# Kernel tuning notes

Hardware: AMD Instinct MI355X
Metric: run time of the kernel (lower is better)

## Reference

```python
import jax, jax.numpy as jnp
import numpy as np

B, SQ, SK, H, NH = 2, 2048, 2048, 2048, 16
HD = H // NH  # 128
NEG = -1e9


def setup_inputs() -> dict:
    key = jax.random.key(0)
    ks = jax.random.split(key, 8)
    hidden_states = jax.random.normal(ks[0], (B, SQ, H), dtype=jnp.float32)
    # key already transposed/expanded for baddbmm: [B*nh, head_dim, key_len]
    k = jax.random.normal(ks[1], (B * NH, HD, SK), dtype=jnp.float32)
    v = jax.random.normal(ks[2], (B, NH, SK, HD), dtype=jnp.float32)
    # additive float causal mask [B, 1, Sq, Sk]
    causal = jnp.tril(jnp.ones((SQ, SK), dtype=bool))
    attention_mask = jnp.where(causal, 0.0, NEG).astype(jnp.float32)
    attention_mask = jnp.broadcast_to(attention_mask[None, None], (B, 1, SQ, SK))
    w_q = jax.random.normal(ks[3], (H, H), dtype=jnp.float32) * 0.02
    b_q = jnp.zeros((H,), dtype=jnp.float32)
    w_proj = jax.random.normal(ks[4], (H, H), dtype=jnp.float32) * 0.02
    b_proj = jnp.zeros((H,), dtype=jnp.float32)
    return {
        "hidden_states": hidden_states,
        "key": k,
        "value": v,
        "attention_mask": attention_mask,
        "w_q": w_q,
        "b_q": b_q,
        "w_proj": w_proj,
        "b_proj": b_proj,
    }


def reference(hidden_states, key, value, attention_mask, w_q, b_q, w_proj, b_proj):
    dtype = hidden_states.dtype
    scale = 1.0 / (HD ** 0.5)  # scale_attn_weights=True, attention_multiplier=None
    # q projection: [B, Sq, H] -> [B, nh, Sq, hd]
    q = hidden_states @ w_q.T + b_q
    q = q.reshape(B, SQ, NH, HD).transpose(0, 2, 1, 3)
    # key comes in as [B*nh, hd, Sk]
    k = key.reshape(B, NH, HD, SK)
    # scores = mask + scale * q @ k  (baddbmm with beta=1)
    scores = attention_mask + scale * jnp.einsum("bhqd,bhdk->bhqk", q, k)
    # softmax in fp32 (attention_softmax_in_fp32=True), cast back
    probs = jax.nn.softmax(scores.astype(jnp.float32), axis=-1).astype(dtype)
    # attn_pdrop=0 -> no dropout
    out = jnp.einsum("bhqk,bhkd->bhqd", probs, value)  # [B, nh, Sq, hd]
    out = out.transpose(0, 2, 1, 3).reshape(B, SQ, H)
    out = out @ w_proj.T + b_proj  # resid_pdrop=0 -> no dropout
    return out
```

## Files before the change

kernel.cpp:

```cpp
#include <hip/hip_runtime.h>
#include <hip/hip_bf16.h>

typedef __bf16 bf16;
typedef __bf16 bf16x4 __attribute__((ext_vector_type(4)));
typedef __bf16 bf16x8 __attribute__((ext_vector_type(8)));
typedef float  f32x4  __attribute__((ext_vector_type(4)));
typedef float  f32x16 __attribute__((ext_vector_type(16)));
typedef unsigned int u32;

#define B_   2
#define SQ_  2048
#define SK_  2048
#define H_   2048
#define NH_  16
#define HD_  128
#define BH_  (B_*NH_)

__device__ inline void gl_lds16(const bf16* g, bf16* l) {
  __builtin_amdgcn_global_load_lds(
      (const __attribute__((address_space(1))) u32*)(const void*)g,
      (__attribute__((address_space(3))) u32*)(void*)l,
      16, 0, 0);
}

__device__ inline float exp2_fast(float x) {
  float r; asm("v_exp_f32 %0, %1" : "=v"(r) : "v"(x)); return r;
}

union PW { u32 w[4]; bf16x8 v; };

__global__ __launch_bounds__(256) void cvt3_f32_bf16(const float* __restrict__ a, bf16* __restrict__ ao,
                                                     const float* __restrict__ b, bf16* __restrict__ bo,
                                                     const float* __restrict__ c, bf16* __restrict__ co) {
  const int blk = blockIdx.x;
  const float* in; bf16* out; int n4, bstart, nblk;
  if (blk < 1024)      { in = a; out = ao; n4 = (B_ * SQ_ * H_) / 4; bstart = 0;    nblk = 1024; }
  else if (blk < 1536) { in = b; out = bo; n4 = (H_ * H_) / 4;       bstart = 1024; nblk = 512; }
  else                 { in = c; out = co; n4 = (H_ * H_) / 4;       bstart = 1536; nblk = 512; }
  int i = (blk - bstart) * 256 + threadIdx.x;
  const int stride = nblk * 256;
  for (; i < n4; i += stride) {
    float4 v = ((const float4*)in)[i];
    bf16x4 w; w[0] = (bf16)v.x; w[1] = (bf16)v.y; w[2] = (bf16)v.z; w[3] = (bf16)v.w;
    ((bf16x4*)out)[i] = w;
  }
}

__global__ __launch_bounds__(256) void transpose_cvt2(const float* __restrict__ key,
                                                      const float* __restrict__ value,
                                                      bf16* __restrict__ kout,
                                                      bf16* __restrict__ vout) {
  __shared__ float tile[64][65];
  const int id = blockIdx.x;
  const float* src; bf16* dst; int R, C, r0, c0, bh;
  if (id < 2048) {
    src = key; dst = kout; R = HD_; C = SK_;
    c0 = (id & 31) * 64; r0 = ((id >> 5) & 1) * 64; bh = id >> 6;
  } else {
    const int j = id - 2048;
    src = value; dst = vout; R = SK_; C = HD_;
    c0 = (j & 1) * 64; r0 = ((j >> 1) & 31) * 64; bh = j >> 6;
  }
  src += (size_t)bh * R * C;
  dst += (size_t)bh * R * C;
  const int t = threadIdx.x;
  const int tx = t & 15, ty = t >> 4;
#pragma unroll
  for (int p = 0; p < 4; ++p) {
    int rr = ty + p * 16;
    float4 v = *(const float4*)&src[(size_t)(r0 + rr) * C + c0 + tx * 4];
    tile[rr][tx * 4 + 0] = v.x; tile[rr][tx * 4 + 1] = v.y;
    tile[rr][tx * 4 + 2] = v.z; tile[rr][tx * 4 + 3] = v.w;
  }
  __syncthreads();
#pragma unroll
  for (int p = 0; p < 4; ++p) {
    int cc = ty + p * 16;
    bf16x4 w;
#pragma unroll
    for (int i = 0; i < 4; ++i) w[i] = (bf16)tile[tx * 4 + i][cc];
    *(bf16x4*)&dst[(size_t)(c0 + cc) * R + r0 + tx * 4] = w;
  }
}

template <typename OutT>
__global__ __launch_bounds__(256) void gemm_bt(const bf16* __restrict__ A,
                                               const bf16* __restrict__ Bw,
                                               const float* __restrict__ bias,
                                               OutT* __restrict__ C,
                                               int M, int N, int K, float osc) {
  __shared__ bf16 Abuf[128 * 32];
  __shared__ bf16 Bbuf[128 * 32];
  const int nbn = N >> 7;
  int wg = blockIdx.x, nwg = gridDim.x;
  int swz = (nwg & 7) ? wg : ((wg & 7) * (nwg >> 3) + (wg >> 3));
  int bm = swz / nbn, bn = swz % nbn;
  const int t = threadIdx.x, lane = t & 63, wid = t >> 6;
  const int r = lane & 15, g = lane >> 4;
  const int wr = wid >> 1, wc = wid & 1;
  const size_t m0 = (size_t)bm * 128, n0 = (size_t)bn * 128;

  f32x4 acc[4][4];
#pragma unroll
  for (int m = 0; m < 4; ++m)
#pragma unroll
    for (int n = 0; n < 4; ++n) acc[m][n] = (f32x4){0.f, 0.f, 0.f, 0.f};

  for (int k0 = 0; k0 < K; k0 += 32) {
    __syncthreads();
#pragma unroll
    for (int p = 0; p < 2; ++p) {
      int c = p * 256 + t;
      int row = c >> 2, off = c & 3;
      gl_lds16(A + (m0 + row) * K + k0 + off * 8, &Abuf[(p * 256 + wid * 64) * 8]);
      gl_lds16(Bw + (n0 + row) * K + k0 + off * 8, &Bbuf[(p * 256 + wid * 64) * 8]);
    }
    __syncthreads();
    bf16x8 af[4], bfr[4];
#pragma unroll
    for (int m = 0; m < 4; ++m)
      af[m] = *(const bf16x8*)&Abuf[(wr * 64 + m * 16 + r) * 32 + g * 8];
#pragma unroll
    for (int n = 0; n < 4; ++n)
      bfr[n] = *(const bf16x8*)&Bbuf[(wc * 64 + n * 16 + r) * 32 + g * 8];
#pragma unroll
    for (int m = 0; m < 4; ++m)
#pragma unroll
      for (int n = 0; n < 4; ++n)
        acc[m][n] = __builtin_amdgcn_mfma_f32_16x16x32_bf16(af[m], bfr[n], acc[m][n], 0, 0, 0);
  }

  float bv[4];
#pragma unroll
  for (int n = 0; n < 4; ++n) bv[n] = bias[n0 + wc * 64 + n * 16 + r];
#pragma unroll
  for (int m = 0; m < 4; ++m)
#pragma unroll
    for (int n = 0; n < 4; ++n)
#pragma unroll
      for (int rr = 0; rr < 4; ++rr) {
        size_t row = m0 + wr * 64 + m * 16 + g * 4 + rr;
        size_t col = n0 + wc * 64 + n * 16 + r;
        C[row * N + col] = (OutT)((acc[m][n][rr] + bv[n]) * osc);
      }
}

__global__ __launch_bounds__(256, 2) void flash_attn(const bf16* __restrict__ Q,
                                                     const bf16* __restrict__ Kt,
                                                     const bf16* __restrict__ Vt,
                                                     bf16* __restrict__ O,
                                                     bf16* __restrict__ part,
                                                     float2* __restrict__ mlbuf) {
  __shared__ bf16 Klds[2][64 * 128];
  __shared__ bf16 Vlds[3][64 * 128];

  const int id = blockIdx.x;
  const int pr = (id >> 3) & 7;
  const int hf = (id >> 6) & 1;
  const int bh = (id & 7) + 8 * (id >> 7);
  const int qtA = 15 - pr, qtB = pr;
  const int nA = 2 * qtA + 2, nB = 2 * qtB + 2;
  const int b = bh >> 4, h = bh & 15;
  const int t = threadIdx.x, lane = t & 63, wid = t >> 6;
  const int l5 = lane & 31, hiL = lane >> 5;

  const bf16* Kbase = Kt + (size_t)bh * SK_ * HD_;
  const bf16* Vbase = Vt + (size_t)bh * HD_ * SK_;

  u32 kSrc[4], vSrc[4];
#pragma unroll
  for (int p = 0; p < 4; ++p) {
    int c = p * 256 + t;
    { int row = c >> 4, off = c & 15, src = off ^ (row & 15);
      kSrc[p] = (u32)(row * HD_ + src * 8); }
    { int srow = c >> 4, j = c & 15, gj = j ^ (srow & 15);
      int d = srow * 2 + (gj >> 3);
      vSrc[p] = (u32)(d * SK_ + (gj & 7) * 8); }
  }

  const int npass = hf ? 2 : 1;
#pragma unroll 1
  for (int ps = 0; ps < npass; ++ps) {
    int qt, lo, hi, partial;
    if (!hf)          { qt = qtA; lo = 0;  hi = 17; partial = 1; }
    else if (ps == 0) { qt = qtA; lo = 17; hi = nA; partial = 1; }
    else              { qt = qtB; lo = 0;  hi = nB; partial = 0; }
    const int qbw = qt * 128 + wid * 32;
    const int q_lane = qbw + l5;

    bf16x8 qf[8];
    {
      const size_t qrow = (size_t)(b * SQ_ + q_lane) * H_ + (size_t)h * HD_;
#pragma unroll
      for (int dt = 0; dt < 8; ++dt)
        qf[dt] = *(const bf16x8*)&Q[qrow + dt * 16 + 8 * hiL];
    }

    f32x16 acc[4];
#pragma unroll
    for (int n = 0; n < 4; ++n)
#pragma unroll
      for (int e = 0; e < 16; ++e) acc[n][e] = 0.f;
    float mrun = -3.0e38f, lpart = 0.f;

    bf16x8 paP[4];
    bool have_prev = false;
    int kc = 0, vp = 2, vc = 0, vn = 1;

    __syncthreads();
    {
      const size_t ks = (size_t)lo * (64 * HD_), vs = (size_t)lo * 64;
#pragma unroll
      for (int p = 0; p < 4; ++p) {
        gl_lds16(Kbase + ks + kSrc[p], &Klds[0][(p * 256 + wid * 64) * 8]);
        gl_lds16(Vbase + vs + vSrc[p], &Vlds[0][(p * 256 + wid * 64) * 8]);
      }
    }
    asm volatile("s_waitcnt vmcnt(0)" ::: "memory");
    __syncthreads();

#pragma unroll 1
    for (int st = lo; st < hi; ++st) {
      if (st + 1 < hi) {
        const size_t ks = (size_t)(st + 1) * (64 * HD_), vs = (size_t)(st + 1) * 64;
#pragma unroll
        for (int p = 0; p < 4; ++p) {
          gl_lds16(Kbase + ks + kSrc[p], &Klds[kc ^ 1][(p * 256 + wid * 64) * 8]);
          gl_lds16(Vbase + vs + vSrc[p], &Vlds[vn][(p * 256 + wid * 64) * 8]);
        }
      }
      const int s0 = st * 64;
      const bool act = (s0 <= qbw + 31);

      f32x16 sv0, sv1;
      if (act) {
#pragma unroll
        for (int e = 0; e < 16; ++e) { sv0[e] = 0.f; sv1[e] = 0.f; }
        __builtin_amdgcn_s_setprio(1);
#pragma unroll
        for (int dt = 0; dt < 8; ++dt) {
          const int dch = ((2 * dt + hiL) ^ (l5 & 15)) * 8;
          bf16x8 kf0 = *(const bf16x8*)&Klds[kc][l5 * 128 + dch];
          bf16x8 kf1 = *(const bf16x8*)&Klds[kc][(32 + l5) * 128 + dch];
          sv0 = __builtin_amdgcn_mfma_f32_32x32x16_bf16(kf0, qf[dt], sv0, 0, 0, 0);
          sv1 = __builtin_amdgcn_mfma_f32_32x32x16_bf16(kf1, qf[dt], sv1, 0, 0, 0);
        }
        __builtin_amdgcn_s_setprio(0);
      }

      if (have_prev) {
        const bf16* vbuf = &Vlds[vp][0];
        __builtin_amdgcn_s_setprio(1);
#pragma unroll
        for (int n = 0; n < 4; ++n) {
          const int sr = n * 16 + (l5 >> 1);
#pragma unroll
          for (int kt = 0; kt < 4; ++kt) {
            const int jj = ((((l5 & 1) << 3) | (2 * kt + hiL)) ^ (l5 >> 1));
            bf16x8 vf = *(const bf16x8*)&vbuf[sr * 128 + jj * 8];
            acc[n] = __builtin_amdgcn_mfma_f32_32x32x16_bf16(paP[kt], vf, acc[n], 0, 0, 0);
          }
        }
        __builtin_amdgcn_s_setprio(0);
        have_prev = false;
      }

      if (act) {
        if (s0 + 63 > qbw) {
#pragma unroll
          for (int r2 = 0; r2 < 16; ++r2) {
            const int kl = (r2 & 3) + 8 * (r2 >> 2) + 4 * hiL;
            if (s0 + kl > q_lane)      sv0[r2] = -3.0e38f;
            if (s0 + 32 + kl > q_lane) sv1[r2] = -3.0e38f;
          }
        }

        float pm = -3.0e38f;
#pragma unroll
        for (int r2 = 0; r2 < 16; ++r2) pm = fmaxf(pm, fmaxf(sv0[r2], sv1[r2]));
        pm = fmaxf(pm, __shfl_xor(pm, 32));
        if (!__all(pm <= mrun + 10.0f ? 1 : 0)) {
          const float mnew = fmaxf(mrun, pm);
          const float corr = exp2_fast(mrun - mnew);
          mrun = mnew; lpart *= corr;
          const int cb = __float_as_int(corr);
#pragma unroll
          for (int r2 = 0; r2 < 16; ++r2) {
            const int q2 = (r2 & 3) + 8 * (r2 >> 2) + 4 * hiL;
            const float cc = __int_as_float(__builtin_amdgcn_ds_bpermute(q2 * 4, cb));
#pragma unroll
            for (int n = 0; n < 4; ++n) acc[n][r2] *= cc;
          }
        }

        float psum = 0.f;
#pragma unroll
        for (int r2 = 0; r2 < 16; ++r2) {
          sv0[r2] = exp2_fast(sv0[r2] - mrun); psum += sv0[r2];
          sv1[r2] = exp2_fast(sv1[r2] - mrun); psum += sv1[r2];
        }
        lpart += psum;

#pragma unroll
        for (int h2 = 0; h2 < 2; ++h2) {
          u32 pk[8], px[8];
#pragma unroll
          for (int j = 0; j < 8; ++j) {
            union { bf16 hh[2]; u32 u; } tt;
            float plo = h2 ? sv1[2 * j] : sv0[2 * j];
            float phi = h2 ? sv1[2 * j + 1] : sv0[2 * j + 1];
            tt.hh[0] = (bf16)plo; tt.hh[1] = (bf16)phi;
            pk[j] = tt.u;
          }
#pragma unroll
          for (int j = 0; j < 8; ++j) px[j] = (u32)__shfl_xor((int)pk[j], 32);
          PW a0, a1;
          a0.w[0] = hiL ? px[2] : pk[0]; a0.w[1] = hiL ? px[3] : pk[1];
          a0.w[2] = hiL ? pk[2] : px[0]; a0.w[3] = hiL ? pk[3] : px[1];
          a1.w[0] = hiL ? px[6] : pk[4]; a1.w[1] = hiL ? px[7] : pk[5];
          a1.w[2] = hiL ? pk[6] : px[4]; a1.w[3] = hiL ? pk[7] : px[5];
          paP[2 * h2]     = a0.v;
          paP[2 * h2 + 1] = a1.v;
        }
        have_prev = true;
      }

      asm volatile("s_waitcnt vmcnt(0)" ::: "memory");
      __syncthreads();
      kc ^= 1;
      const int ovp = vp; vp = vc; vc = vn; vn = ovp;
    }

    if (have_prev) {
      const bf16* vbuf = &Vlds[vp][0];
#pragma unroll
      for (int n = 0; n < 4; ++n) {
        const int sr = n * 16 + (l5 >> 1);
#pragma unroll
        for (int kt = 0; kt < 4; ++kt) {
          const int jj = ((((l5 & 1) << 3) | (2 * kt + hiL)) ^ (l5 >> 1));
          bf16x8 vf = *(const bf16x8*)&vbuf[sr * 128 + jj * 8];
          acc[n] = __builtin_amdgcn_mfma_f32_32x32x16_bf16(paP[kt], vf, acc[n], 0, 0, 0);
        }
      }
      have_prev = false;
    }

    float ltot = lpart + __shfl_xor(lpart, 32);
    if (partial) {
      const int slot = (hf * 8 + pr) * 32 + bh;
      bf16* pbase = part + (size_t)slot * (128 * 128);
#pragma unroll
      for (int n = 0; n < 4; ++n)
#pragma unroll
        for (int r2 = 0; r2 < 16; ++r2) {
          const int rowt = wid * 32 + (r2 & 3) + 8 * (r2 >> 2) + 4 * hiL;
          pbase[rowt * 128 + n * 32 + l5] = (bf16)acc[n][r2];
        }
      if (lane < 32)
        mlbuf[(size_t)slot * 128 + wid * 32 + lane] = float2{mrun, ltot};
    } else {
      const float inv = 1.0f / ltot;
      const int ib = __float_as_int(inv);
#pragma unroll
      for (int r2 = 0; r2 < 16; ++r2) {
        const int q2 = (r2 & 3) + 8 * (r2 >> 2) + 4 * hiL;
        const float ic = __int_as_float(__builtin_amdgcn_ds_bpermute(q2 * 4, ib));
        const size_t rowg = (size_t)(b * SQ_ + qbw + q2);
#pragma unroll
        for (int n = 0; n < 4; ++n)
          O[rowg * H_ + (size_t)h * HD_ + n * 32 + l5] = (bf16)(acc[n][r2] * ic);
      }
    }
  }
}

__global__ __launch_bounds__(256) void flash_merge(const bf16* __restrict__ part,
                                                   const float2* __restrict__ mlbuf,
                                                   bf16* __restrict__ O) {
  const int gid = blockIdx.x * 256 + threadIdx.x;
  const int idx = gid >> 4;
  const int d8 = (gid & 15) * 8;
  const int row = idx & 127;
  const int bh = (idx >> 7) & 31;
  const int pr = idx >> 12;
  const int qtA = 15 - pr;
  const int b = bh >> 4, h = bh & 15;
  const int slot0 = pr * 32 + bh;
  const int slot1 = (8 + pr) * 32 + bh;
  const float2 ml0 = mlbuf[(size_t)slot0 * 128 + row];
  const float2 ml1 = mlbuf[(size_t)slot1 * 128 + row];
  const float M = fmaxf(ml0.x, ml1.x);
  const float c0 = exp2_fast(ml0.x - M);
  const float c1 = exp2_fast(ml1.x - M);
  const float inv = 1.0f / (c0 * ml0.y + c1 * ml1.y);
  const bf16x8 a0 = *(const bf16x8*)&part[(size_t)slot0 * (128 * 128) + row * 128 + d8];
  const bf16x8 a1 = *(const bf16x8*)&part[(size_t)slot1 * (128 * 128) + row * 128 + d8];
  bf16x8 o;
#pragma unroll
  for (int j = 0; j < 8; ++j)
    o[j] = (bf16)((c0 * (float)a0[j] + c1 * (float)a1[j]) * inv);
  const size_t orow = (size_t)(b * SQ_ + qtA * 128 + row);
  *(bf16x8*)&O[orow * H_ + (size_t)h * HD_ + d8] = o;
}

extern "C" void kernel_launch(void* const* d_in, const int* in_sizes, int n_in,
                              void* d_out, int out_size, void* d_ws, size_t ws_size,
                              hipStream_t stream) {
  const float* hidden = (const float*)d_in[0];
  const float* key    = (const float*)d_in[1];
  const float* value  = (const float*)d_in[2];
  const float* w_q    = (const float*)d_in[4];
  const float* b_q    = (const float*)d_in[5];
  const float* w_proj = (const float*)d_in[6];
  const float* b_proj = (const float*)d_in[7];
  float* out = (float*)d_out;

  const size_t N_HID = (size_t)B_ * SQ_ * H_;
  const size_t N_W   = (size_t)H_ * H_;
  const size_t N_KV  = (size_t)BH_ * SK_ * HD_;
  const float SC2 = 0.08838834764831845f * 1.4426950408889634f;

  bf16* hid_bf  = (bf16*)d_ws;
  bf16* wq_bf   = hid_bf + N_HID;
  bf16* wp_bf   = wq_bf + N_W;
  bf16* k_bf    = wp_bf + N_W;
  bf16* vt_bf   = k_bf + N_KV;
  bf16* q_bf    = vt_bf + N_KV;
  bf16* part_bf = q_bf + N_HID;
  float2* ml_bf = (float2*)(part_bf + (size_t)512 * 128 * 128);
  bf16* attn_bf = hid_bf;

  cvt3_f32_bf16<<<2048, 256, 0, stream>>>(hidden, hid_bf, w_q, wq_bf, w_proj, wp_bf);
  transpose_cvt2<<<4096, 256, 0, stream>>>(key, value, k_bf, vt_bf);

  gemm_bt<bf16><<<(B_ * SQ_ / 128) * (H_ / 128), 256, 0, stream>>>(
      hid_bf, wq_bf, b_q, q_bf, B_ * SQ_, H_, H_, SC2);

  flash_attn<<<512, 256, 0, stream>>>(q_bf, k_bf, vt_bf, attn_bf, part_bf, ml_bf);
  flash_merge<<<2048, 256, 0, stream>>>(part_bf, ml_bf, attn_bf);

  gemm_bt<float><<<(B_ * SQ_ / 128) * (H_ / 128), 256, 0, stream>>>(
      attn_bf, wp_bf, b_proj, out, B_ * SQ_, H_, H_, 1.0f);
}
```

Measured before the change: 211.3 us.

## Triple-buffer GEMM LDS loads with XOR swizzle and merge prepass kernels

The bf16 GEMM now keeps three LDS stages and issues global-to-LDS loads two k-tiles ahead. It replaces the per-iteration double sync with a vmcnt wait plus a single barrier, and raises wave priority around the MFMA block. LDS rows are XOR-swizzled to cut bank conflicts on fragment reads. The two conversion/transpose kernels are also fused into one launch to save launch overhead, at the cost of triple the GEMM LDS footprint (48KB), which may lower occupancy.

```diff
diff --git a/kernel.cpp b/kernel.cpp
--- a/kernel.cpp
+++ b/kernel.cpp
@@ -29,41 +29,40 @@
 
 union PW { u32 w[4]; bf16x8 v; };
 
-__global__ __launch_bounds__(256) void cvt3_f32_bf16(const float* __restrict__ a, bf16* __restrict__ ao,
-                                                     const float* __restrict__ b, bf16* __restrict__ bo,
-                                                     const float* __restrict__ c, bf16* __restrict__ co) {
-  const int blk = blockIdx.x;
-  const float* in; bf16* out; int n4, bstart, nblk;
-  if (blk < 1024)      { in = a; out = ao; n4 = (B_ * SQ_ * H_) / 4; bstart = 0;    nblk = 1024; }
-  else if (blk < 1536) { in = b; out = bo; n4 = (H_ * H_) / 4;       bstart = 1024; nblk = 512; }
-  else                 { in = c; out = co; n4 = (H_ * H_) / 4;       bstart = 1536; nblk = 512; }
-  int i = (blk - bstart) * 256 + threadIdx.x;
-  const int stride = nblk * 256;
-  for (; i < n4; i += stride) {
-    float4 v = ((const float4*)in)[i];
-    bf16x4 w; w[0] = (bf16)v.x; w[1] = (bf16)v.y; w[2] = (bf16)v.z; w[3] = (bf16)v.w;
-    ((bf16x4*)out)[i] = w;
-  }
-}
-
-__global__ __launch_bounds__(256) void transpose_cvt2(const float* __restrict__ key,
-                                                      const float* __restrict__ value,
-                                                      bf16* __restrict__ kout,
-                                                      bf16* __restrict__ vout) {
+__global__ __launch_bounds__(256) void prepass(const float* __restrict__ hidden, bf16* __restrict__ hid,
+                                               const float* __restrict__ wq, bf16* __restrict__ wqo,
+                                               const float* __restrict__ wp, bf16* __restrict__ wpo,
+                                               const float* __restrict__ key, const float* __restrict__ value,
+                                               bf16* __restrict__ kout, bf16* __restrict__ vout) {
   __shared__ float tile[64][65];
   const int id = blockIdx.x;
+  const int t = threadIdx.x;
+  if (id < 2048) {
+    const float* in; bf16* out; int n4, bstart, nblk;
+    if (id < 1024)      { in = hidden; out = hid; n4 = (B_ * SQ_ * H_) / 4; bstart = 0;    nblk = 1024; }
+    else if (id < 1536) { in = wq;     out = wqo; n4 = (H_ * H_) / 4;       bstart = 1024; nblk = 512; }
+    else                { in = wp;     out = wpo; n4 = (H_ * H_) / 4;       bstart = 1536; nblk = 512; }
+    int i = (id - bstart) * 256 + t;
+    const int stride = nblk * 256;
+    for (; i < n4; i += stride) {
+      float4 v = ((const float4*)in)[i];
+      bf16x4 w; w[0] = (bf16)v.x; w[1] = (bf16)v.y; w[2] = (bf16)v.z; w[3] = (bf16)v.w;
+      ((bf16x4*)out)[i] = w;
+    }
+    return;
+  }
+  const int j0 = id - 2048;
   const float* src; bf16* dst; int R, C, r0, c0, bh;
-  if (id < 2048) {
+  if (j0 < 2048) {
     src = key; dst = kout; R = HD_; C = SK_;
-    c0 = (id & 31) * 64; r0 = ((id >> 5) & 1) * 64; bh = id >> 6;
+    c0 = (j0 & 31) * 64; r0 = ((j0 >> 5) & 1) * 64; bh = j0 >> 6;
   } else {
-    const int j = id - 2048;
+    const int j = j0 - 2048;
     src = value; dst = vout; R = SK_; C = HD_;
     c0 = (j & 1) * 64; r0 = ((j >> 1) & 31) * 64; bh = j >> 6;
   }
   src += (size_t)bh * R * C;
   dst += (size_t)bh * R * C;
-  const int t = threadIdx.x;
   const int tx = t & 15, ty = t >> 4;
 #pragma unroll
   for (int p = 0; p < 4; ++p) {
@@ -89,8 +88,8 @@
                                                const float* __restrict__ bias,
                                                OutT* __restrict__ C,
                                                int M, int N, int K, float osc) {
-  __shared__ bf16 Abuf[128 * 32];
-  __shared__ bf16 Bbuf[128 * 32];
+  __shared__ bf16 Abuf[3][128 * 32];
+  __shared__ bf16 Bbuf[3][128 * 32];
   const int nbn = N >> 7;
   int wg = blockIdx.x, nwg = gridDim.x;
   int swz = (nwg & 7) ? wg : ((wg & 7) * (nwg >> 3) + (wg >> 3));
@@ -100,34 +99,63 @@
   const int wr = wid >> 1, wc = wid & 1;
   const size_t m0 = (size_t)bm * 128, n0 = (size_t)bn * 128;
 
+  u32 sOff[2];
+#pragma unroll
+  for (int p = 0; p < 2; ++p) {
+    int c = p * 256 + t, row = c >> 2, off = c & 3, src = off ^ (row & 3);
+    sOff[p] = (u32)(row * K + src * 8);
+  }
+  const bf16* Ab = A + m0 * K;
+  const bf16* Bb = Bw + n0 * K;
+
   f32x4 acc[4][4];
 #pragma unroll
   for (int m = 0; m < 4; ++m)
 #pragma unroll
     for (int n = 0; n < 4; ++n) acc[m][n] = (f32x4){0.f, 0.f, 0.f, 0.f};
 
-  for (int k0 = 0; k0 < K; k0 += 32) {
-    __syncthreads();
+  const int nk = K >> 5;
+#pragma unroll
+  for (int kt = 0; kt < 2; ++kt)
 #pragma unroll
     for (int p = 0; p < 2; ++p) {
-      int c = p * 256 + t;
-      int row = c >> 2, off = c & 3;
-      gl_lds16(A + (m0 + row) * K + k0 + off * 8, &Abuf[(p * 256 + wid * 64) * 8]);
-      gl_lds16(Bw + (n0 + row) * K + k0 + off * 8, &Bbuf[(p * 256 + wid * 64) * 8]);
-    }
-    __syncthreads();
+      gl_lds16(Ab + kt * 32 + sOff[p], &Abuf[kt][(p * 256 + wid * 64) * 8]);
+      gl_lds16(Bb + kt * 32 + sOff[p], &Bbuf[kt][(p * 256 + wid * 64) * 8]);
+    }
+  asm volatile("s_waitcnt vmcnt(4)" ::: "memory");
+  __syncthreads();
+
+#pragma unroll 1
+  for (int kt = 0; kt < nk; ++kt) {
+    const int cur = kt % 3;
+    if (kt + 2 < nk) {
+      const int nb = (kt + 2) % 3;
+      const int k0 = (kt + 2) * 32;
+#pragma unroll
+      for (int p = 0; p < 2; ++p) {
+        gl_lds16(Ab + k0 + sOff[p], &Abuf[nb][(p * 256 + wid * 64) * 8]);
+        gl_lds16(Bb + k0 + sOff[p], &Bbuf[nb][(p * 256 + wid * 64) * 8]);
+      }
+    }
     bf16x8 af[4], bfr[4];
 #pragma unroll
     for (int m = 0; m < 4; ++m)
-      af[m] = *(const bf16x8*)&Abuf[(wr * 64 + m * 16 + r) * 32 + g * 8];
+      af[m] = *(const bf16x8*)&Abuf[cur][(wr * 64 + m * 16 + r) * 32 + ((g ^ (r & 3)) * 8)];
 #pragma unroll
     for (int n = 0; n < 4; ++n)
-      bfr[n] = *(const bf16x8*)&Bbuf[(wc * 64 + n * 16 + r) * 32 + g * 8];
+      bfr[n] = *(const bf16x8*)&Bbuf[cur][(wc * 64 + n * 16 + r) * 32 + ((g ^ (r & 3)) * 8)];
+    __builtin_amdgcn_s_setprio(1);
 #pragma unroll
     for (int m = 0; m < 4; ++m)
 #pragma unroll
       for (int n = 0; n < 4; ++n)
         acc[m][n] = __builtin_amdgcn_mfma_f32_16x16x32_bf16(af[m], bfr[n], acc[m][n], 0, 0, 0);
+    __builtin_amdgcn_s_setprio(0);
+    if (kt + 2 < nk)
+      asm volatile("s_waitcnt vmcnt(4)" ::: "memory");
+    else
+      asm volatile("s_waitcnt vmcnt(0)" ::: "memory");
+    __syncthreads();
   }
 
   float bv[4];
@@ -431,8 +459,8 @@
   float2* ml_bf = (float2*)(part_bf + (size_t)512 * 128 * 128);
   bf16* attn_bf = hid_bf;
 
-  cvt3_f32_bf16<<<2048, 256, 0, stream>>>(hidden, hid_bf, w_q, wq_bf, w_proj, wp_bf);
-  transpose_cvt2<<<4096, 256, 0, stream>>>(key, value, k_bf, vt_bf);
+  prepass<<<6144, 256, 0, stream>>>(hidden, hid_bf, w_q, wq_bf, w_proj, wp_bf,
+                                    key, value, k_bf, vt_bf);
 
   gemm_bt<bf16><<<(B_ * SQ_ / 128) * (H_ / 128), 256, 0, stream>>>(
       hid_bf, wq_bf, b_q, q_bf, B_ * SQ_, H_, H_, SC2);
```

After: 203.3 us (median of 2 runs). -3.8%, faster.
